# Optimization experiments

Measured on AMD Instinct MI355X. Metric: run time of the kernel, lower is better.

The kernel has to match this reference:

```python
import jax, jax.numpy as jnp
import numpy as np

B, G, K, N, M, E, L = 8, 512, 64, 1024, 128, 4, 5

def _lin(x, w, b):
    return x @ w.T + b

def setup_inputs():
    key = jax.random.key(0)
    ks = jax.random.split(key, 20)
    def nrm(k, shape, s=1.0):
        return jax.random.normal(k, shape, dtype=jnp.float32) * s
    def lin_p(k, out_d, in_d):
        k1, k2 = jax.random.split(k)
        s = 1.0 / float(np.sqrt(in_d))
        return nrm(k1, (out_d, in_d), s), nrm(k2, (out_d,), s)
    inp = {}
    inp["z"] = nrm(ks[0], (B, G, K, M), 0.5)
    inp["hs_grid"] = nrm(ks[1], (B, G, M))
    inp["hs_key"] = nrm(ks[2], (B, K, M))
    inp["lig_rep"] = nrm(ks[3], (B, E))
    inp["hs_rec"] = nrm(ks[4], (B, N, M))
    inp["w_Rl"] = jnp.ones((1,), dtype=jnp.float32)
    inp["w_mask"] = jax.random.randint(ks[5], (B, K), 0, 2)
    dims = {"wra": (M, M), "wrh": (M, M), "wla": (M, M), "wlh": (M, M),
            "z1": (1, M), "wcR": (M, M), "wcl": (M, M), "kR": (M, M),
            "mapL": (L, 2 * M + E), "fin": (1, L)}
    for i, nm in enumerate(dims):
        w, b = lin_p(ks[6 + i], *dims[nm])
        inp[nm + "_w"] = w
        inp[nm + "_b"] = b
    return inp

def reference(z, hs_grid, hs_key, lig_rep, hs_rec, w_Rl, w_mask,
              wra_w, wra_b, wrh_w, wrh_b, wla_w, wla_b, wlh_w, wlh_b,
              z1_w, z1_b, wcR_w, wcR_b, wcl_w, wcl_b, kR_w, kR_b,
              mapL_w, mapL_b, fin_w, fin_b):
    exp_z = jnp.exp(z)                                    # [B,G,K,M]
    zr = exp_z / exp_z.sum(axis=-2, keepdims=True)        # pseudo-softmax over K
    ra = jnp.einsum('bgkm,bkm->bgm', zr, hs_key)          # [B,G,M]
    zl = exp_z / exp_z.sum(axis=-3, keepdims=True)        # pseudo-softmax over G
    la = jnp.einsum('bgkm,bgm->bkm', zl, hs_grid)         # [B,K,M]
    ra_rh = _lin(ra, wra_w, wra_b) + _lin(hs_grid, wrh_w, wrh_b)  # [B,G,M]
    la_lh = _lin(la, wla_w, wla_b) + _lin(hs_key, wlh_w, wlh_b)   # [B,K,M]
    att = _lin(z, z1_w, z1_b)[..., 0]                     # [B,G,K]
    att_l = jax.nn.softmax(att, axis=2).sum(axis=1)       # [B,K]
    att_r = jax.nn.softmax(att, axis=1).sum(axis=2)       # [B,G]
    key_rep = jnp.einsum('bk,bkm->bm', att_l, la_lh)      # [B,M]
    grid_rep = jnp.einsum('bg,bgm->bm', att_r, ra_rh)     # [B,M]
    Rh = _lin(hs_rec, wcR_w, wcR_b)                       # [B,N,M]
    lh = _lin(hs_key, wcl_w, wcl_b)                       # [B,K,M]
    z_Rl = jnp.einsum('bnh,bkh->bnk', Rh, lh)             # [B,N,K]
    masked = jnp.where(w_mask[:, None, :] == 0, jnp.float32(-1e10), w_Rl * z_Rl)
    z_Rl = jax.nn.softmax(masked, axis=1)                 # softmax over N
    kfr = jnp.einsum('bnk,bnh->bkh', z_Rl, hs_rec)        # [B,K,M]
    kfr = _lin(kfr, kR_w, kR_b)
    kfr = jnp.einsum('bk,bkh->bh', att_l, kfr)            # [B,M]
    key_rep = key_rep + kfr
    pair_rep = jnp.concatenate([key_rep, lig_rep, grid_rep], axis=1)  # [B,2M+E]
    pair_rep = _lin(pair_rep, mapL_w, mapL_b)             # [B,L]
    return _lin(pair_rep, fin_w, fin_b)[..., 0]           # [B]
```

## Files before the change

### kernel.cpp

```cpp
#include <hip/hip_runtime.h>

#define Bb 8
#define Gg 512
#define Kk 64
#define Nn 1024
#define Mm 128
#define KM (Kk * Mm)
#define GPB 16
#define NCH (Gg / GPB)

struct P7 { const float* p[7]; };

__global__ __launch_bounds__(1024) void kA(
    const float* __restrict__ z, const float* __restrict__ hs_grid,
    const float* __restrict__ hs_key, const float* __restrict__ z1w,
    P7 ptrs, float* __restrict__ wT,
    float* __restrict__ raOut, float* __restrict__ attOut,
    float* __restrict__ laNum, float* __restrict__ laDen)
{
  __shared__ __align__(16) float smem[18432];
  const int bid = blockIdx.x;
  const int t = threadIdx.x;

  if (bid >= Bb * NCH) {
    float* tile = smem;
    const int r = bid - Bb * NCH;
    const int mat = r >> 4, tl = r & 15;
    const int xo = (tl & 3) * 32, y0 = (tl >> 2) * 32;
    const int tx = t & 31, ty = t >> 5;
    const float* src = ptrs.p[mat];
    float* dst = wT + (size_t)mat * Mm * Mm;
    tile[ty * 33 + tx] = src[(size_t)(y0 + ty) * Mm + xo + tx];
    __syncthreads();
    dst[(size_t)(xo + ty) * Mm + y0 + tx] = tile[tx * 33 + ty];
    return;
  }

  float* s_hskey  = smem;
  float* s_hsgrid = smem + 8192;
  float* s_rn     = smem + 10240;
  float* s_rd     = smem + 14336;

  const int b = bid >> 5;
  const int gblk = bid & 31;
  const int lane_m = t & 31;
  const int m4 = lane_m << 2;
  const int kgrp = t >> 5;
  const int wv = t >> 6;

  const float* hkb = hs_key + (size_t)b * KM;
  for (int idx = t; idx < KM; idx += 1024) s_hskey[idx] = hkb[idx];
  const float* hgb = hs_grid + ((size_t)b * Gg + gblk * GPB) * Mm;
  for (int idx = t; idx < GPB * Mm; idx += 1024) s_hsgrid[idx] = hgb[idx];

  const float zw0 = z1w[m4], zw1 = z1w[m4 + 1], zw2 = z1w[m4 + 2], zw3 = z1w[m4 + 3];

  float la_n[2][4], la_d[2][4];
#pragma unroll
  for (int i = 0; i < 2; ++i)
#pragma unroll
    for (int j = 0; j < 4; ++j) { la_n[i][j] = 0.f; la_d[i][j] = 0.f; }

  const float* zb = z + ((size_t)b * Gg + gblk * GPB) * (size_t)Mm * Kk;
  const int ofs0 = (kgrp * 2) * Mm + m4;
  const int ofs1 = ofs0 + Mm;
  float4 c0 = *reinterpret_cast<const float4*>(zb + ofs0);
  float4 c1 = *reinterpret_cast<const float4*>(zb + ofs1);

  __syncthreads();

  for (int gl = 0; gl < GPB; ++gl) {
    float4 n0 = c0, n1 = c1;
    if (gl < GPB - 1) {
      n0 = *reinterpret_cast<const float4*>(zb + (size_t)(gl + 1) * KM + ofs0);
      n1 = *reinterpret_cast<const float4*>(zb + (size_t)(gl + 1) * KM + ofs1);
    }
    const int g = gblk * GPB + gl;
    const float4 hg = *reinterpret_cast<const float4*>(s_hsgrid + gl * Mm + m4);
    float rn0 = 0, rn1 = 0, rn2 = 0, rn3 = 0, rd0 = 0, rd1 = 0, rd2 = 0, rd3 = 0;
#pragma unroll
    for (int i = 0; i < 2; ++i) {
      const float4 v = (i == 0) ? c0 : c1;
      const int k = kgrp * 2 + i;
      const float e0 = __expf(v.x), e1 = __expf(v.y), e2 = __expf(v.z), e3 = __expf(v.w);
      la_n[i][0] += e0 * hg.x; la_n[i][1] += e1 * hg.y; la_n[i][2] += e2 * hg.z; la_n[i][3] += e3 * hg.w;
      la_d[i][0] += e0;        la_d[i][1] += e1;        la_d[i][2] += e2;        la_d[i][3] += e3;
      const float4 hk = *reinterpret_cast<const float4*>(s_hskey + k * Mm + m4);
      rn0 += e0 * hk.x; rn1 += e1 * hk.y; rn2 += e2 * hk.z; rn3 += e3 * hk.w;
      rd0 += e0; rd1 += e1; rd2 += e2; rd3 += e3;
      float ap = v.x * zw0 + v.y * zw1 + v.z * zw2 + v.w * zw3;
      ap += __shfl_xor(ap, 16); ap += __shfl_xor(ap, 8); ap += __shfl_xor(ap, 4);
      ap += __shfl_xor(ap, 2);  ap += __shfl_xor(ap, 1);
      if (lane_m == 0) attOut[((size_t)b * Gg + g) * Kk + k] = ap;
    }
    rn0 += __shfl_xor(rn0, 32); rn1 += __shfl_xor(rn1, 32); rn2 += __shfl_xor(rn2, 32); rn3 += __shfl_xor(rn3, 32);
    rd0 += __shfl_xor(rd0, 32); rd1 += __shfl_xor(rd1, 32); rd2 += __shfl_xor(rd2, 32); rd3 += __shfl_xor(rd3, 32);
    float* rnB = s_rn + (gl & 1) * 2048;
    float* rdB = s_rd + (gl & 1) * 2048;
    if ((t & 63) < 32) {
      *reinterpret_cast<float4*>(rnB + wv * Mm + m4) = make_float4(rn0, rn1, rn2, rn3);
      *reinterpret_cast<float4*>(rdB + wv * Mm + m4) = make_float4(rd0, rd1, rd2, rd3);
    }
    __syncthreads();
    if (t < Mm) {
      float num = 0.f, den = 0.f;
#pragma unroll
      for (int ww = 0; ww < 16; ++ww) { num += rnB[ww * Mm + t]; den += rdB[ww * Mm + t]; }
      raOut[((size_t)b * Gg + g) * Mm + t] = num / den;
    }
    c0 = n0; c1 = n1;
  }

  const size_t base = ((size_t)(b * NCH + gblk)) * KM;
#pragma unroll
  for (int i = 0; i < 2; ++i) {
    const int k = kgrp * 2 + i;
    *reinterpret_cast<float4*>(laNum + base + k * Mm + m4) =
        make_float4(la_n[i][0], la_n[i][1], la_n[i][2], la_n[i][3]);
    *reinterpret_cast<float4*>(laDen + base + k * Mm + m4) =
        make_float4(la_d[i][0], la_d[i][1], la_d[i][2], la_d[i][3]);
  }
}

__global__ __launch_bounds__(256) void kB(
    const float* __restrict__ laNum, const float* __restrict__ laDen, float* __restrict__ la,
    const float* __restrict__ att, float* __restrict__ attlP,
    float* __restrict__ attrPM, float* __restrict__ attrPS,
    const float* __restrict__ hs_key, const float* __restrict__ wT,
    const float* __restrict__ wcR_w, const float* __restrict__ wcl_b,
    float* __restrict__ Lk)
{
  __shared__ __align__(16) float smem[1088];
  const int bid = blockIdx.x;
  const int t = threadIdx.x;

  if (bid < 256) {
    const int idx = bid * 256 + t;
    const int b = idx >> 13, r = idx & 8191;
    const float* np = laNum + (size_t)b * NCH * KM + r;
    const float* dp = laDen + (size_t)b * NCH * KM + r;
    float num = 0.f, den = 0.f;
#pragma unroll 8
    for (int p = 0; p < NCH; ++p) { num += np[(size_t)p * KM]; den += dp[(size_t)p * KM]; }
    la[idx] = num / den;
  } else if (bid < 320) {
    const int blk = bid - 256;
    const int b = blk >> 3, p = blk & 7;
    const int w = t >> 6, lane = t & 63;
    float acc = 0.f;
    for (int j = 0; j < 16; ++j) {
      const int g = p * 64 + w * 16 + j;
      const float a = att[((size_t)b * Gg + g) * Kk + lane];
      float mx = a;
      for (int off = 32; off; off >>= 1) mx = fmaxf(mx, __shfl_xor(mx, off));
      const float e = __expf(a - mx);
      float s = e;
      for (int off = 32; off; off >>= 1) s += __shfl_xor(s, off);
      acc += e / s;
    }
    float* sred = smem;
    sred[w * 64 + lane] = acc;
    __syncthreads();
    if (t < 64) attlP[(b * 8 + p) * 64 + t] = sred[t] + sred[64 + t] + sred[128 + t] + sred[192 + t];
  } else if (bid < 384) {
    const int blk = bid - 320;
    const int b = blk >> 3, gc = blk & 7;
    const int k = t & 63, j4 = t >> 6;
    float m = -1e30f, s = 0.f;
    for (int j = 0; j < 16; ++j) {
      const int g = gc * 64 + j4 * 16 + j;
      const float a = att[((size_t)b * Gg + g) * Kk + k];
      if (a > m) { s = s * __expf(m - a) + 1.0f; m = a; }
      else s += __expf(a - m);
    }
    float* sm = smem;
    float* ss = smem + 256;
    sm[j4 * 64 + k] = m; ss[j4 * 64 + k] = s;
    __syncthreads();
    if (t < 64) {
      float M = sm[t];
      for (int q = 1; q < 4; ++q) M = fmaxf(M, sm[q * 64 + t]);
      float S = 0.f;
      for (int q = 0; q < 4; ++q) S += ss[q * 64 + t] * __expf(sm[q * 64 + t] - M);
      attrPM[(b * 8 + gc) * 64 + t] = M;
      attrPS[(b * 8 + gc) * 64 + t] = S;
    }
  } else {
    const int blk = bid - 384;
    const int b = blk >> 3, k8 = blk & 7;
    float* s_lh = smem;
    const int m = t & 127;
    const int half = __builtin_amdgcn_readfirstlane(t >> 7);
    const float* wclT = wT + 5 * 16384;
    {
      const float* keyb = hs_key + ((size_t)b * Kk + k8 * 8 + half * 4) * Mm;
      float a0 = 0.f, a1 = 0.f, a2 = 0.f, a3 = 0.f;
      for (int h = 0; h < 128; ++h) {
        const float w = wclT[(size_t)h * Mm + m];
        const float r0v = keyb[h];
        const float r1v = keyb[128 + h];
        const float r2v = keyb[256 + h];
        const float r3v = keyb[384 + h];
        a0 += r0v * w; a1 += r1v * w; a2 += r2v * w; a3 += r3v * w;
      }
      const float bm = wcl_b[m];
      s_lh[(half * 4 + 0) * 132 + m] = a0 + bm;
      s_lh[(half * 4 + 1) * 132 + m] = a1 + bm;
      s_lh[(half * 4 + 2) * 132 + m] = a2 + bm;
      s_lh[(half * 4 + 3) * 132 + m] = a3 + bm;
    }
    __syncthreads();
    {
      const int h = m;
      const int r0 = half * 4;
      float b0 = 0.f, b1 = 0.f, b2 = 0.f, b3 = 0.f;
      for (int mq = 0; mq < 32; ++mq) {
        const float4 L0 = *reinterpret_cast<const float4*>(&s_lh[(r0 + 0) * 132 + mq * 4]);
        const float4 L1 = *reinterpret_cast<const float4*>(&s_lh[(r0 + 1) * 132 + mq * 4]);
        const float4 L2 = *reinterpret_cast<const float4*>(&s_lh[(r0 + 2) * 132 + mq * 4]);
        const float4 L3 = *reinterpret_cast<const float4*>(&s_lh[(r0 + 3) * 132 + mq * 4]);
        const float w0 = wcR_w[(size_t)(mq * 4 + 0) * Mm + h];
        const float w1 = wcR_w[(size_t)(mq * 4 + 1) * Mm + h];
        const float w2 = wcR_w[(size_t)(mq * 4 + 2) * Mm + h];
        const float w3 = wcR_w[(size_t)(mq * 4 + 3) * Mm + h];
        b0 += L0.x * w0 + L0.y * w1 + L0.z * w2 + L0.w * w3;
        b1 += L1.x * w0 + L1.y * w1 + L1.z * w2 + L1.w * w3;
        b2 += L2.x * w0 + L2.y * w1 + L2.z * w2 + L2.w * w3;
        b3 += L3.x * w0 + L3.y * w1 + L3.z * w2 + L3.w * w3;
      }
      const size_t ob = ((size_t)b * Kk + k8 * 8 + r0) * Mm + h;
      Lk[ob] = b0; Lk[ob + Mm] = b1; Lk[ob + 2 * Mm] = b2; Lk[ob + 3 * Mm] = b3;
    }
  }
}

__global__ __launch_bounds__(256) void kC(
    const float* __restrict__ att, const float* __restrict__ attrPM, const float* __restrict__ attrPS,
    float* __restrict__ att_r,
    const float* __restrict__ hs_rec, const float* __restrict__ Lk,
    const int* __restrict__ mask, const float* __restrict__ wRl,
    float* __restrict__ scores, float* __restrict__ pmT, float* __restrict__ psT)
{
  __shared__ __align__(16) float smem[4608];
  const int bid = blockIdx.x;
  const int t = threadIdx.x;

  if (bid < 64) {
    const int b = bid >> 3, gc = bid & 7;
    const int k = t & 63, grp = t >> 6;
    float* Mx = smem;
    float* S = smem + 64;
    if (t < 64) {
      float M = -1e30f;
      for (int p = 0; p < 8; ++p) M = fmaxf(M, attrPM[(b * 8 + p) * 64 + t]);
      float s = 0.f;
      for (int p = 0; p < 8; ++p) s += attrPS[(b * 8 + p) * 64 + t] * __expf(attrPM[(b * 8 + p) * 64 + t] - M);
      Mx[t] = M; S[t] = s;
    }
    __syncthreads();
    const float Mk = Mx[k], Sk = S[k];
    for (int j = 0; j < 16; ++j) {
      const int g = gc * 64 + grp * 16 + j;
      float p = __expf(att[((size_t)b * Gg + g) * Kk + k] - Mk) / Sk;
      for (int off = 32; off; off >>= 1) p += __shfl_xor(p, off);
      if (k == 0) att_r[b * Gg + g] = p;
    }
  } else {
    const int vb = bid - 64;
    const int b = vb >> 6, ntile = vb & 63;
    const int n0 = ntile * 16;
    const int k = t & 63;
    const int hq = __builtin_amdgcn_readfirstlane(t >> 6);
    float rLk[32];
    {
      const float* Lp = Lk + ((size_t)b * Kk + k) * Mm + hq * 32;
#pragma unroll
      for (int j = 0; j < 8; ++j) {
        const float4 v = *reinterpret_cast<const float4*>(Lp + j * 4);
        rLk[j * 4 + 0] = v.x; rLk[j * 4 + 1] = v.y;
        rLk[j * 4 + 2] = v.z; rLk[j * 4 + 3] = v.w;
      }
    }
    float acc[16];
    const float* rb = hs_rec + ((size_t)b * Nn + n0) * Mm + hq * 32;
#pragma unroll
    for (int r = 0; r < 16; ++r) {
      const float* rp = rb + r * Mm;
      float s = 0.f;
#pragma unroll
      for (int j = 0; j < 32; ++j) s += rp[j] * rLk[j];
      acc[r] = s;
    }
    float* s_acc = smem;
    float* s_m   = smem + 4096;
    float* s_s   = smem + 4352;
#pragma unroll
    for (int r = 0; r < 16; ++r) s_acc[(hq * 16 + r) * 64 + k] = acc[r];
    __syncthreads();
    const float wv = wRl[0];
    const bool msk = (mask[b * Kk + k] == 0);
    float m = -3.0e38f, ssum = 0.f;
    for (int q = 0; q < 4; ++q) {
      const int idx = q * 256 + t;
      const int r = idx >> 6, kk = idx & 63;
      float v = s_acc[r * 64 + kk] + s_acc[(16 + r) * 64 + kk] +
                s_acc[(32 + r) * 64 + kk] + s_acc[(48 + r) * 64 + kk];
      v = msk ? -1e10f : wv * v;
      scores[((size_t)b * Nn + n0 + r) * Kk + kk] = v;
      if (v > m) { ssum = ssum * __expf(m - v) + 1.0f; m = v; }
      else ssum += __expf(v - m);
    }
    s_m[hq * 64 + k] = m; s_s[hq * 64 + k] = ssum;
    __syncthreads();
    if (t < 64) {
      float M = fmaxf(fmaxf(s_m[t], s_m[64 + t]), fmaxf(s_m[128 + t], s_m[192 + t]));
      float S = 0.f;
#pragma unroll
      for (int q = 0; q < 4; ++q) S += s_s[q * 64 + t] * __expf(s_m[q * 64 + t] - M);
      pmT[((size_t)b * 64 + ntile) * 64 + t] = M;
      psT[((size_t)b * 64 + ntile) * 64 + t] = S;
    }
  }
}

__global__ __launch_bounds__(512) void kD(
    const float* __restrict__ scores, const float* __restrict__ hs_rec,
    const float* __restrict__ pmT, const float* __restrict__ psT,
    const float* __restrict__ attlP, const float* __restrict__ att_r,
    const float* __restrict__ ra, const float* __restrict__ hs_grid,
    const float* __restrict__ la, const float* __restrict__ hs_key,
    float* __restrict__ uP, float* __restrict__ w1P, float* __restrict__ w2P,
    float* __restrict__ w0P, float* __restrict__ v1, float* __restrict__ v2,
    float* __restrict__ sAv)
{
  __shared__ float sm[1280];
  __shared__ float s_attl[64];
  __shared__ float sM[64], sSi[64];
  const int bid = blockIdx.x;
  const int t = threadIdx.x;

  if (bid < 64) {
    const int b = bid >> 3, nc = bid & 7;
    if (t < 64) {
      float a = 0.f;
      for (int p = 0; p < 8; ++p) a += attlP[(b * 8 + p) * 64 + t];
      s_attl[t] = a;
      float M = -3.0e38f;
      for (int nt = 0; nt < 64; ++nt) M = fmaxf(M, pmT[((size_t)b * 64 + nt) * 64 + t]);
      float S = 0.f;
      for (int nt = 0; nt < 64; ++nt)
        S += psT[((size_t)b * 64 + nt) * 64 + t] * __expf(pmT[((size_t)b * 64 + nt) * 64 + t] - M);
      sM[t] = M; sSi[t] = 1.0f / S;
    }
    __syncthreads();
    const int n = t >> 2, ks = t & 3;
    const float* sc = scores + ((size_t)b * Nn + nc * 128 + n) * Kk + ks * 16;
    float qp = 0.f;
#pragma unroll
    for (int j = 0; j < 16; ++j) {
      const int k = ks * 16 + j;
      qp += s_attl[k] * __expf(sc[j] - sM[k]) * sSi[k];
    }
    sm[n * 4 + ks] = qp;
    __syncthreads();
    float* q = sm + 512;
    if (t < 128) q[t] = sm[t * 4] + sm[t * 4 + 1] + sm[t * 4 + 2] + sm[t * 4 + 3];
    __syncthreads();
    const int h = t & 127, nq = t >> 7;
    float acc = 0.f;
    const float* hr = hs_rec + ((size_t)b * Nn + nc * 128 + nq * 32) * Mm + h;
    for (int j = 0; j < 32; ++j) acc += q[nq * 32 + j] * hr[(size_t)j * Mm];
    float* red = sm + 640;
    red[nq * 128 + h] = acc;
    __syncthreads();
    if (t < 128) uP[((size_t)b * 8 + nc) * 128 + t] = red[t] + red[128 + t] + red[256 + t] + red[384 + t];
  } else if (bid < 128) {
    const int blk = bid - 64;
    const int b = blk >> 3, gc = blk & 7;
    float* s_ar = sm + 1152;
    if (t < 64) s_ar[t] = att_r[b * Gg + gc * 64 + t];
    __syncthreads();
    const int h = t & 127, gq = t >> 7;
    float a1 = 0.f, a2 = 0.f;
    const float* rp = ra + ((size_t)b * Gg + gc * 64 + gq * 16) * Mm + h;
    const float* gp = hs_grid + ((size_t)b * Gg + gc * 64 + gq * 16) * Mm + h;
    for (int j = 0; j < 16; ++j) {
      const float w = s_ar[gq * 16 + j];
      a1 += w * rp[(size_t)j * Mm];
      a2 += w * gp[(size_t)j * Mm];
    }
    float* r1 = sm;
    float* r2 = sm + 512;
    r1[gq * 128 + h] = a1; r2[gq * 128 + h] = a2;
    __syncthreads();
    if (t < 128) {
      w1P[((size_t)b * 8 + gc) * 128 + t] = r1[t] + r1[128 + t] + r1[256 + t] + r1[384 + t];
      w2P[((size_t)b * 8 + gc) * 128 + t] = r2[t] + r2[128 + t] + r2[256 + t] + r2[384 + t];
    }
    if (t == 0) {
      float s = 0.f;
      for (int j = 0; j < 64; ++j) s += s_ar[j];
      w0P[b * 8 + gc] = s;
    }
  } else {
    const int b = bid - 128;
    if (t < 64) {
      float a = 0.f;
      for (int p = 0; p < 8; ++p) a += attlP[(b * 8 + p) * 64 + t];
      s_attl[t] = a;
    }
    __syncthreads();
    const int h = t & 127, kq = t >> 7;
    float a1 = 0.f, a2 = 0.f;
    const float* lp = la + ((size_t)b * Kk + kq * 16) * Mm + h;
    const float* kp = hs_key + ((size_t)b * Kk + kq * 16) * Mm + h;
    for (int j = 0; j < 16; ++j) {
      const float w = s_attl[kq * 16 + j];
      a1 += w * lp[(size_t)j * Mm];
      a2 += w * kp[(size_t)j * Mm];
    }
    float* r1 = sm;
    float* r2 = sm + 512;
    r1[kq * 128 + h] = a1; r2[kq * 128 + h] = a2;
    __syncthreads();
    if (t < 128) {
      v1[b * 128 + t] = r1[t] + r1[128 + t] + r1[256 + t] + r1[384 + t];
      v2[b * 128 + t] = r2[t] + r2[128 + t] + r2[256 + t] + r2[384 + t];
    }
    if (t == 0) {
      float s = 0.f;
      for (int j = 0; j < 64; ++j) s += s_attl[j];
      sAv[b] = s;
    }
  }
}

__global__ __launch_bounds__(256) void kE(
    const float* __restrict__ uP, const float* __restrict__ w1P, const float* __restrict__ w2P,
    const float* __restrict__ w0P, const float* __restrict__ v1, const float* __restrict__ v2,
    const float* __restrict__ sAv, const float* __restrict__ wT,
    const float* __restrict__ wra_b, const float* __restrict__ wrh_b,
    const float* __restrict__ wla_b, const float* __restrict__ wlh_b,
    const float* __restrict__ kR_b, const float* __restrict__ lig_rep,
    const float* __restrict__ mapL_w, const float* __restrict__ mapL_b,
    const float* __restrict__ fin_w, const float* __restrict__ fin_b,
    float* __restrict__ out)
{
  __shared__ float sV1[128], sV2[128], sU[128], sW1[128], sW2[128];
  __shared__ float sPair[260];
  __shared__ float sRed[2][2][128];
  __shared__ float s5[8];
  __shared__ float sSc[2];
  const int b = blockIdx.x, t = threadIdx.x;
  const int m = t & 127, hf = t >> 7;

  if (t < 128) {
    float u = 0.f, w1 = 0.f, w2 = 0.f;
    for (int c = 0; c < 8; ++c) {
      u  += uP[((size_t)b * 8 + c) * 128 + t];
      w1 += w1P[((size_t)b * 8 + c) * 128 + t];
      w2 += w2P[((size_t)b * 8 + c) * 128 + t];
    }
    sU[t] = u; sW1[t] = w1; sW2[t] = w2;
    sV1[t] = v1[b * 128 + t]; sV2[t] = v2[b * 128 + t];
  }
  if (t == 0) {
    float s = 0.f;
    for (int c = 0; c < 8; ++c) s += w0P[b * 8 + c];
    sSc[0] = s;
    sSc[1] = sAv[b];
  }
  __syncthreads();

  const float* wraT = wT;
  const float* wrhT = wT + 1 * 16384;
  const float* wlaT = wT + 2 * 16384;
  const float* wlhT = wT + 3 * 16384;
  const float* kRT  = wT + 6 * 16384;
  float key = 0.f, grd = 0.f;
  for (int h = hf * 64; h < hf * 64 + 64; ++h) {
    key += sV1[h] * wlaT[h * Mm + m] + sV2[h] * wlhT[h * Mm + m] + sU[h] * kRT[h * Mm + m];
    grd += sW1[h] * wraT[h * Mm + m] + sW2[h] * wrhT[h * Mm + m];
  }
  sRed[0][hf][m] = key; sRed[1][hf][m] = grd;
  __syncthreads();
  if (t < 128) {
    const float sR = sSc[0], sA = sSc[1];
    sPair[t] = sRed[0][0][t] + sRed[0][1][t] + sA * (wla_b[t] + wlh_b[t] + kR_b[t]);
    sPair[132 + t] = sRed[1][0][t] + sRed[1][1][t] + sR * (wra_b[t] + wrh_b[t]);
  }
  if (t < 4) sPair[128 + t] = lig_rep[b * 4 + t];
  __syncthreads();

  const int wv = t >> 6, lane = t & 63;
  for (int l = wv; l < 5; l += 4) {
    float acc = 0.f;
    for (int c = lane; c < 260; c += 64) acc += sPair[c] * mapL_w[l * 260 + c];
    for (int off = 32; off; off >>= 1) acc += __shfl_xor(acc, off);
    if (lane == 0) s5[l] = acc + mapL_b[l];
  }
  __syncthreads();
  if (t == 0) {
    float o = fin_b[0];
    for (int l = 0; l < 5; ++l) o += s5[l] * fin_w[l];
    out[b] = o;
  }
}

extern "C" void kernel_launch(void* const* d_in, const int* in_sizes, int n_in,
                              void* d_out, int out_size, void* d_ws, size_t ws_size,
                              hipStream_t stream) {
  const float* z       = (const float*)d_in[0];
  const float* hs_grid = (const float*)d_in[1];
  const float* hs_key  = (const float*)d_in[2];
  const float* lig_rep = (const float*)d_in[3];
  const float* hs_rec  = (const float*)d_in[4];
  const float* w_Rl    = (const float*)d_in[5];
  const int*   w_mask  = (const int*)d_in[6];
  const float* wra_w = (const float*)d_in[7];  const float* wra_b = (const float*)d_in[8];
  const float* wrh_w = (const float*)d_in[9];  const float* wrh_b = (const float*)d_in[10];
  const float* wla_w = (const float*)d_in[11]; const float* wla_b = (const float*)d_in[12];
  const float* wlh_w = (const float*)d_in[13]; const float* wlh_b = (const float*)d_in[14];
  const float* z1_w  = (const float*)d_in[15];
  const float* wcR_w = (const float*)d_in[17]; const float* wcR_b = (const float*)d_in[18];
  const float* wcl_w = (const float*)d_in[19]; const float* wcl_b = (const float*)d_in[20];
  const float* kR_w  = (const float*)d_in[21]; const float* kR_b  = (const float*)d_in[22];
  const float* mapL_w = (const float*)d_in[23]; const float* mapL_b = (const float*)d_in[24];
  const float* fin_w  = (const float*)d_in[25]; const float* fin_b  = (const float*)d_in[26];
  float* out = (float*)d_out;

  float* w = (float*)d_ws;
  float* wT    = w;
  float* ra    = wT + 7 * 16384;
  float* att   = ra + Bb * Gg * Mm;
  float* laNum = att + Bb * Gg * Kk;
  float* laDen = laNum + Bb * NCH * Kk * Mm;
  float* la    = laDen + Bb * NCH * Kk * Mm;
  float* attlP = la + Bb * Kk * Mm;
  float* attrPM = attlP + Bb * 8 * 64;
  float* attrPS = attrPM + Bb * 8 * 64;
  float* att_r = attrPS + Bb * 8 * 64;
  float* Lk    = att_r + Bb * Gg;
  float* scores = Lk + Bb * Kk * Mm;

  float* pmT  = laNum;
  float* psT  = laNum + 32768;
  float* uP   = laNum + 65536;
  float* w1P  = laNum + 73728;
  float* w2P  = laNum + 81920;
  float* w0P  = laNum + 90112;
  float* v1   = laNum + 90176;
  float* v2   = laNum + 91200;
  float* sAv  = laNum + 92224;

  P7 ptrs;
  ptrs.p[0] = wra_w; ptrs.p[1] = wrh_w; ptrs.p[2] = wla_w; ptrs.p[3] = wlh_w;
  ptrs.p[4] = wcR_w; ptrs.p[5] = wcl_w; ptrs.p[6] = kR_w;

  kA<<<Bb * NCH + 112, 1024, 0, stream>>>(z, hs_grid, hs_key, z1_w, ptrs, wT,
                                          ra, att, laNum, laDen);
  kB<<<448, 256, 0, stream>>>(laNum, laDen, la, att, attlP, attrPM, attrPS,
                              hs_key, wT, wcR_w, wcl_b, Lk);
  kC<<<576, 256, 0, stream>>>(att, attrPM, attrPS, att_r, hs_rec, Lk,
                              w_mask, w_Rl, scores, pmT, psT);
  kD<<<136, 512, 0, stream>>>(scores, hs_rec, pmT, psT, attlP, att_r,
                              ra, hs_grid, la, hs_key,
                              uP, w1P, w2P, w0P, v1, v2, sAv);
  kE<<<Bb, 256, 0, stream>>>(uP, w1P, w2P, w0P, v1, v2, sAv, wT,
                             wra_b, wrh_b, wla_b, wlh_b, kR_b, lig_rep,
                             mapL_w, mapL_b, fin_w, fin_b, out);
}
```

Baseline: 91.59 us.

## Hold hs_key in registers, vectorize loads, widen final reduction kernel

In kA, each thread now keeps its two hs_key rows in registers instead of staging the whole 64x128 hs_key tile in shared memory. This shrinks shared memory from 72KB to 40KB, which may raise occupancy and removes a load phase. The wcl and hs_rec dot-product loops in kB and kC switch to float4 vectorized loads. kE moves from 256 to 1024 threads with an 8-way split of the h reduction, so each thread makes fewer serial weight loads, at the cost of an extra shared reduction.

```diff
diff --git a/kernel.cpp b/kernel.cpp
--- a/kernel.cpp
+++ b/kernel.cpp
@@ -7,7 +7,7 @@
 #define Mm 128
 #define KM (Kk * Mm)
 #define GPB 16
-#define NCH (Gg / GPB)
+#define NCH 32
 
 struct P7 { const float* p[7]; };
 
@@ -18,7 +18,7 @@
     float* __restrict__ raOut, float* __restrict__ attOut,
     float* __restrict__ laNum, float* __restrict__ laDen)
 {
-  __shared__ __align__(16) float smem[18432];
+  __shared__ __align__(16) float smem[10240];
   const int bid = blockIdx.x;
   const int t = threadIdx.x;
 
@@ -36,10 +36,9 @@
     return;
   }
 
-  float* s_hskey  = smem;
-  float* s_hsgrid = smem + 8192;
-  float* s_rn     = smem + 10240;
-  float* s_rd     = smem + 14336;
+  float* s_hsgrid = smem;
+  float* s_rn     = smem + 2048;
+  float* s_rd     = smem + 6144;
 
   const int b = bid >> 5;
   const int gblk = bid & 31;
@@ -48,22 +47,23 @@
   const int kgrp = t >> 5;
   const int wv = t >> 6;
 
-  const float* hkb = hs_key + (size_t)b * KM;
-  for (int idx = t; idx < KM; idx += 1024) s_hskey[idx] = hkb[idx];
   const float* hgb = hs_grid + ((size_t)b * Gg + gblk * GPB) * Mm;
   for (int idx = t; idx < GPB * Mm; idx += 1024) s_hsgrid[idx] = hgb[idx];
 
-  const float zw0 = z1w[m4], zw1 = z1w[m4 + 1], zw2 = z1w[m4 + 2], zw3 = z1w[m4 + 3];
-
-  float la_n[2][4], la_d[2][4];
-#pragma unroll
-  for (int i = 0; i < 2; ++i)
-#pragma unroll
-    for (int j = 0; j < 4; ++j) { la_n[i][j] = 0.f; la_d[i][j] = 0.f; }
-
-  const float* zb = z + ((size_t)b * Gg + gblk * GPB) * (size_t)Mm * Kk;
   const int ofs0 = (kgrp * 2) * Mm + m4;
   const int ofs1 = ofs0 + Mm;
+  const float4 hk0 = *reinterpret_cast<const float4*>(hs_key + (size_t)b * KM + ofs0);
+  const float4 hk1 = *reinterpret_cast<const float4*>(hs_key + (size_t)b * KM + ofs1);
+
+  const float zw0 = z1w[m4], zw1 = z1w[m4 + 1], zw2 = z1w[m4 + 2], zw3 = z1w[m4 + 3];
+
+  float la_n[2][4], la_d[2][4];
+#pragma unroll
+  for (int i = 0; i < 2; ++i)
+#pragma unroll
+    for (int j = 0; j < 4; ++j) { la_n[i][j] = 0.f; la_d[i][j] = 0.f; }
+
+  const float* zb = z + ((size_t)b * Gg + gblk * GPB) * (size_t)KM;
   float4 c0 = *reinterpret_cast<const float4*>(zb + ofs0);
   float4 c1 = *reinterpret_cast<const float4*>(zb + ofs1);
 
@@ -81,11 +81,11 @@
 #pragma unroll
     for (int i = 0; i < 2; ++i) {
       const float4 v = (i == 0) ? c0 : c1;
+      const float4 hk = (i == 0) ? hk0 : hk1;
       const int k = kgrp * 2 + i;
       const float e0 = __expf(v.x), e1 = __expf(v.y), e2 = __expf(v.z), e3 = __expf(v.w);
       la_n[i][0] += e0 * hg.x; la_n[i][1] += e1 * hg.y; la_n[i][2] += e2 * hg.z; la_n[i][3] += e3 * hg.w;
       la_d[i][0] += e0;        la_d[i][1] += e1;        la_d[i][2] += e2;        la_d[i][3] += e3;
-      const float4 hk = *reinterpret_cast<const float4*>(s_hskey + k * Mm + m4);
       rn0 += e0 * hk.x; rn1 += e1 * hk.y; rn2 += e2 * hk.z; rn3 += e3 * hk.w;
       rd0 += e0; rd1 += e1; rd2 += e2; rd3 += e3;
       float ap = v.x * zw0 + v.y * zw1 + v.z * zw2 + v.w * zw3;
@@ -195,13 +195,19 @@
     {
       const float* keyb = hs_key + ((size_t)b * Kk + k8 * 8 + half * 4) * Mm;
       float a0 = 0.f, a1 = 0.f, a2 = 0.f, a3 = 0.f;
-      for (int h = 0; h < 128; ++h) {
-        const float w = wclT[(size_t)h * Mm + m];
-        const float r0v = keyb[h];
-        const float r1v = keyb[128 + h];
-        const float r2v = keyb[256 + h];
-        const float r3v = keyb[384 + h];
-        a0 += r0v * w; a1 += r1v * w; a2 += r2v * w; a3 += r3v * w;
+      for (int h4 = 0; h4 < 32; ++h4) {
+        const float4 r0v = *reinterpret_cast<const float4*>(keyb + h4 * 4);
+        const float4 r1v = *reinterpret_cast<const float4*>(keyb + 128 + h4 * 4);
+        const float4 r2v = *reinterpret_cast<const float4*>(keyb + 256 + h4 * 4);
+        const float4 r3v = *reinterpret_cast<const float4*>(keyb + 384 + h4 * 4);
+        const float w0 = wclT[(size_t)(h4 * 4 + 0) * Mm + m];
+        const float w1 = wclT[(size_t)(h4 * 4 + 1) * Mm + m];
+        const float w2 = wclT[(size_t)(h4 * 4 + 2) * Mm + m];
+        const float w3 = wclT[(size_t)(h4 * 4 + 3) * Mm + m];
+        a0 += r0v.x * w0 + r0v.y * w1 + r0v.z * w2 + r0v.w * w3;
+        a1 += r1v.x * w0 + r1v.y * w1 + r1v.z * w2 + r1v.w * w3;
+        a2 += r2v.x * w0 + r2v.y * w1 + r2v.z * w2 + r2v.w * w3;
+        a3 += r3v.x * w0 + r3v.y * w1 + r3v.z * w2 + r3v.w * w3;
       }
       const float bm = wcl_b[m];
       s_lh[(half * 4 + 0) * 132 + m] = a0 + bm;
@@ -288,7 +294,11 @@
       const float* rp = rb + r * Mm;
       float s = 0.f;
 #pragma unroll
-      for (int j = 0; j < 32; ++j) s += rp[j] * rLk[j];
+      for (int j4 = 0; j4 < 8; ++j4) {
+        const float4 rv = *reinterpret_cast<const float4*>(rp + j4 * 4);
+        s += rv.x * rLk[j4 * 4] + rv.y * rLk[j4 * 4 + 1] +
+             rv.z * rLk[j4 * 4 + 2] + rv.w * rLk[j4 * 4 + 3];
+      }
       acc[r] = s;
     }
     float* s_acc = smem;
@@ -435,7 +445,7 @@
   }
 }
 
-__global__ __launch_bounds__(256) void kE(
+__global__ __launch_bounds__(1024) void kE(
     const float* __restrict__ uP, const float* __restrict__ w1P, const float* __restrict__ w2P,
     const float* __restrict__ w0P, const float* __restrict__ v1, const float* __restrict__ v2,
     const float* __restrict__ sAv, const float* __restrict__ wT,
@@ -447,8 +457,8 @@
     float* __restrict__ out)
 {
   __shared__ float sV1[128], sV2[128], sU[128], sW1[128], sW2[128];
-  __shared__ float sPair[260];
-  __shared__ float sRed[2][2][128];
+  __shared__ float sPair[264];
+  __shared__ float sRed[2][8][128];
   __shared__ float s5[8];
   __shared__ float sSc[2];
   const int b = blockIdx.x, t = threadIdx.x;
@@ -478,7 +488,7 @@
   const float* wlhT = wT + 3 * 16384;
   const float* kRT  = wT + 6 * 16384;
   float key = 0.f, grd = 0.f;
-  for (int h = hf * 64; h < hf * 64 + 64; ++h) {
+  for (int h = hf * 16; h < hf * 16 + 16; ++h) {
     key += sV1[h] * wlaT[h * Mm + m] + sV2[h] * wlhT[h * Mm + m] + sU[h] * kRT[h * Mm + m];
     grd += sW1[h] * wraT[h * Mm + m] + sW2[h] * wrhT[h * Mm + m];
   }
@@ -486,18 +496,21 @@
   __syncthreads();
   if (t < 128) {
     const float sR = sSc[0], sA = sSc[1];
-    sPair[t] = sRed[0][0][t] + sRed[0][1][t] + sA * (wla_b[t] + wlh_b[t] + kR_b[t]);
-    sPair[132 + t] = sRed[1][0][t] + sRed[1][1][t] + sR * (wra_b[t] + wrh_b[t]);
+    float kk = 0.f, gg = 0.f;
+#pragma unroll
+    for (int q = 0; q < 8; ++q) { kk += sRed[0][q][t]; gg += sRed[1][q][t]; }
+    sPair[t] = kk + sA * (wla_b[t] + wlh_b[t] + kR_b[t]);
+    sPair[132 + t] = gg + sR * (wra_b[t] + wrh_b[t]);
   }
   if (t < 4) sPair[128 + t] = lig_rep[b * 4 + t];
   __syncthreads();
 
-  const int wv = t >> 6, lane = t & 63;
-  for (int l = wv; l < 5; l += 4) {
+  const int wq = t >> 6, lane = t & 63;
+  if (wq < 5) {
     float acc = 0.f;
-    for (int c = lane; c < 260; c += 64) acc += sPair[c] * mapL_w[l * 260 + c];
+    for (int c = lane; c < 260; c += 64) acc += sPair[c] * mapL_w[wq * 260 + c];
     for (int off = 32; off; off >>= 1) acc += __shfl_xor(acc, off);
-    if (lane == 0) s5[l] = acc + mapL_b[l];
+    if (lane == 0) s5[wq] = acc + mapL_b[wq];
   }
   __syncthreads();
   if (t == 0) {
@@ -566,7 +579,7 @@
   kD<<<136, 512, 0, stream>>>(scores, hs_rec, pmT, psT, attlP, att_r,
                               ra, hs_grid, la, hs_key,
                               uP, w1P, w2P, w0P, v1, v2, sAv);
-  kE<<<Bb, 256, 0, stream>>>(uP, w1P, w2P, w0P, v1, v2, sAv, wT,
-                             wra_b, wrh_b, wla_b, wlh_b, kR_b, lig_rep,
-                             mapL_w, mapL_b, fin_w, fin_b, out);
+  kE<<<Bb, 1024, 0, stream>>>(uP, w1P, w2P, w0P, v1, v2, sAv, wT,
+                              wra_b, wrh_b, wla_b, wlh_b, kR_b, lig_rep,
+                              mapL_w, mapL_b, fin_w, fin_b, out);
 }
```

After: 89.06 us (median of 2 runs). -2.8%, faster.
